# Optimization experiments

Measured on AMD Instinct MI355X. Metric: run time of the kernel, lower is better.

The kernel has to match this reference:

```python
import jax, jax.numpy as jnp
import numpy as np

NEG_SLOPE = 0.2
EPS = 1e-9


def setup_inputs() -> dict:
    key = jax.random.key(0)
    ks = jax.random.split(key, 6)
    B, N, E, H, F = 2, 40000, 640000, 4, 32
    X = jax.random.normal(ks[0], (B, N, H, F), dtype=jnp.float32)
    A_self = jax.random.normal(ks[1], (H, F), dtype=jnp.float32)
    A_adjc = jax.random.normal(ks[2], (H, F), dtype=jnp.float32)
    targets = jax.random.randint(ks[3], (B, E), 0, N, dtype=jnp.int32)
    sources = jax.random.randint(ks[4], (B, E), 0, N, dtype=jnp.int32)
    degree = jax.random.uniform(ks[5], (B, E), dtype=jnp.float32)
    return {"X": X, "A_self": A_self, "A_adjc": A_adjc, "degree": degree,
            "targets": targets, "sources": sources, "N": N}


def reference(X, A_self, A_adjc, degree, targets, sources, N):
    # X: [B, N, H, F]; targets/sources: [B, E]
    # per-node attention logits: [B, N, H]
    e_self = jnp.einsum("bnhf,hf->bnh", X, A_self)
    e_adjc = jnp.einsum("bnhf,hf->bnh", X, A_adjc)
    # gather to edges: [B, E, H]
    es = jnp.take_along_axis(e_self, targets[:, :, None], axis=1)
    ea = jnp.take_along_axis(e_adjc, sources[:, :, None], axis=1)
    e = jax.nn.leaky_relu(es + ea, negative_slope=NEG_SLOPE)

    seg_max = jax.vmap(lambda v, i: jax.ops.segment_max(v, i, num_segments=N))
    seg_sum = jax.vmap(lambda v, i: jax.ops.segment_sum(v, i, num_segments=N))

    # exact normalization from source: exp(e - seg_max(e)), then divide by
    # seg_max of the exponentials (+eps), both gathered back to edges.
    m1 = jnp.take_along_axis(seg_max(e, targets), targets[:, :, None], axis=1)
    e = jnp.exp(e - m1)
    m2 = jnp.take_along_axis(seg_max(e, targets), targets[:, :, None], axis=1)
    attn = (e / (m2 + EPS))[..., None]  # [B, E, H, 1]; dropout omitted (eval)

    # message passing: gather source features, weight, scatter-sum to targets
    msg = jnp.take_along_axis(X, sources[:, :, None, None], axis=1) * attn  # [B,E,H,F]
    out = seg_sum(msg, targets)  # [B, N, H, F]
    return out
```

## Files before the change

### kernel.cpp

```cpp
#include <hip/hip_runtime.h>
#include <stdint.h>

#define BB     2
#define NNODE  40000
#define NEDGE  640000
#define NH     4
#define NF     32
#define NHF    128
#define SEGN   (BB * NNODE)
#define GEDGE  (BB * NEDGE)
#define EC     16
#define SLOT   48

#define W      512
#define NBK_B  79
#define NBK    (BB * NBK_B)
#define CAP    9216
#define BLK_E  2048
#define NBLKA  (GEDGE / BLK_E)

static constexpr float NEG_SLOPE = 0.2f;
static constexpr float NEG_BIG   = -3.4e38f;

__global__ void prep_k(const float* __restrict__ X,
                       const float* __restrict__ As,
                       const float* __restrict__ Aa,
                       float* __restrict__ S, float* __restrict__ A,
                       unsigned* __restrict__ cursor) {
    int idx = blockIdx.x * blockDim.x + threadIdx.x;
    if (idx < NBK) cursor[idx] = 0u;
    if (idx >= SEGN * NH) return;
    int h = idx & (NH - 1);
    const float4* xv = (const float4*)(X + (size_t)idx * NF);
    const float4* sv = (const float4*)(As + h * NF);
    const float4* av = (const float4*)(Aa + h * NF);
    float s = 0.f, a = 0.f;
#pragma unroll
    for (int i = 0; i < 8; ++i) {
        float4 x = xv[i];
        float4 ws = sv[i];
        float4 wa = av[i];
        s += x.x * ws.x + x.y * ws.y + x.z * ws.z + x.w * ws.w;
        a += x.x * wa.x + x.y * wa.y + x.z * wa.z + x.w * wa.w;
    }
    S[idx] = s;
    A[idx] = a;
}

__global__ __launch_bounds__(256) void binA_k(const int* __restrict__ tg,
                                              const int* __restrict__ sc,
                                              unsigned* __restrict__ cursor,
                                              unsigned* __restrict__ pairs) {
    __shared__ unsigned hist[NBK];
    __shared__ unsigned lofs[NBK];
    __shared__ unsigned gofs[NBK];
    __shared__ unsigned wsum[4];
    __shared__ unsigned staged[BLK_E];
    __shared__ unsigned char sbk[BLK_E];
    int t = threadIdx.x;
    int base = blockIdx.x * BLK_E;
    for (int i = t; i < NBK; i += 256) hist[i] = 0u;
    __syncthreads();

    unsigned pr[8];
    unsigned short pbk[8], plp[8];
#pragma unroll
    for (int k = 0; k < 8; ++k) {
        int e = base + k * 256 + t;
        int tgv = tg[e], scv = sc[e];
        int b = (e >= NEDGE) ? 1 : 0;
        unsigned bk = (unsigned)(b * NBK_B + (tgv >> 9));
        pr[k]  = ((unsigned)(tgv & (W - 1)) << 16) | (unsigned)scv;
        pbk[k] = (unsigned short)bk;
        plp[k] = (unsigned short)atomicAdd(&hist[bk], 1u);
    }
    __syncthreads();
    {
        int lane = t & 63, w = t >> 6;
        unsigned v = (t < NBK) ? hist[t] : 0u;
        unsigned inc = v;
#pragma unroll
        for (int d = 1; d < 64; d <<= 1) {
            unsigned u = __shfl_up(inc, d);
            if (lane >= d) inc += u;
        }
        if (lane == 63) wsum[w] = inc;
        __syncthreads();
        unsigned woff = 0;
#pragma unroll
        for (int i = 0; i < 3; ++i) { if (i < w) woff += wsum[i]; }
        if (t < NBK) {
            lofs[t] = woff + inc - v;
            if (v > 0u)
                gofs[t] = atomicAdd(&cursor[t], v);
        }
    }
    __syncthreads();
#pragma unroll
    for (int k = 0; k < 8; ++k) {
        unsigned j = lofs[pbk[k]] + plp[k];
        staged[j] = pr[k];
        sbk[j] = (unsigned char)pbk[k];
    }
    __syncthreads();
    for (int j = t; j < BLK_E; j += 256) {
        unsigned bk = sbk[j];
        unsigned dst = gofs[bk] + ((unsigned)j - lofs[bk]);
        if (dst < CAP)
            pairs[(size_t)bk * CAP + dst] = staged[j];
    }
}

__global__ __launch_bounds__(1024) void binB_k(const unsigned* __restrict__ cursor,
                                               const unsigned* __restrict__ pairs,
                                               unsigned short* __restrict__ srt,
                                               unsigned* __restrict__ deg) {
    __shared__ unsigned short loc[W * SLOT];
    __shared__ unsigned dloc[W];
    int t = threadIdx.x;
    int gbk = blockIdx.x;
    int b = gbk / NBK_B;
    int bkloc = gbk - b * NBK_B;
    int node0 = b * NNODE + bkloc * W;
    int wEff = min(W, NNODE - bkloc * W);
    for (int i = t; i < W; i += 1024) dloc[i] = 0u;
    __syncthreads();
    int nE = (int)min(cursor[gbk], (unsigned)CAP);
    const unsigned* pb = pairs + (size_t)gbk * CAP;
    for (int j = t; j < nE; j += 1024) {
        unsigned p = pb[j];
        unsigned tl = p >> 16;
        unsigned pos = atomicAdd(&dloc[tl], 1u);
        if (pos < SLOT)
            loc[tl * SLOT + pos] = (unsigned short)(p & 0xFFFFu);
    }
    __syncthreads();
    unsigned* srt32 = (unsigned*)(srt + (size_t)node0 * SLOT);
    const unsigned* loc32 = (const unsigned*)loc;
    int n32 = wEff * SLOT / 2;
    for (int i = t; i < n32; i += 1024) srt32[i] = loc32[i];
    for (int i = t; i < wEff; i += 1024) deg[node0 + i] = dloc[i];
}

__global__ __launch_bounds__(256) void gather_k(
        const float* __restrict__ X, const float* __restrict__ S,
        const float* __restrict__ A, const unsigned* __restrict__ deg,
        const unsigned short* __restrict__ srt, float* __restrict__ OUT) {
    int node = blockIdx.x * 4 + (threadIdx.x >> 6);
    int t = threadIdx.x & 63;
    int hs = t & 3;
    int es = t >> 2;
    int h32 = t >> 5;
    int q = t & 31;
    int haq = q >> 3;
    int dg = min((int)deg[node], SLOT);
    int bbase = (node >= NNODE) ? NNODE : 0;
    size_t beg = (size_t)node * SLOT;

    float sh = S[node * NH + hs];
    float m_st = NEG_BIG;
    float m_ac = NEG_BIG;
    float4 acc = make_float4(0.f, 0.f, 0.f, 0.f);

    for (int c = 0; c < dg; c += EC) {
        int e = c + es;
        int sb = bbase;
        float v = NEG_BIG;
        if (e < dg) {
            sb = bbase + (int)srt[beg + e];
            v = sh + A[sb * NH + hs];
            v = v > 0.f ? v : NEG_SLOPE * v;
        }
        float m = v;
        m = fmaxf(m, __shfl_xor(m, 4));
        m = fmaxf(m, __shfl_xor(m, 8));
        m = fmaxf(m, __shfl_xor(m, 16));
        m = fmaxf(m, __shfl_xor(m, 32));
        m_st = fmaxf(m_st, m);
        float w = (e < dg) ? __expf(v - m_st) : 0.f;
        float ma_new = fmaxf(m_ac, __shfl(m, haq));
        float r = __expf(m_ac - ma_new);
        m_ac = ma_new;
        acc.x *= r; acc.y *= r; acc.z *= r; acc.w *= r;

        int cend = min(EC, dg - c);
        int npair = (cend + 1) >> 1;
#pragma unroll 8
        for (int i = 0; i < npair; ++i) {
            int e2 = 2 * i + h32;
            float we  = __shfl(w, 4 * e2 + haq);
            int   sbe = __shfl(sb, 4 * e2);
            const float4 x = *(const float4*)(X + (size_t)sbe * NHF + 4 * q);
            acc.x += x.x * we;
            acc.y += x.y * we;
            acc.z += x.z * we;
            acc.w += x.w * we;
        }
    }
    acc.x += __shfl_xor(acc.x, 32);
    acc.y += __shfl_xor(acc.y, 32);
    acc.z += __shfl_xor(acc.z, 32);
    acc.w += __shfl_xor(acc.w, 32);
    if (t < 32) {
        float4* o = (float4*)(OUT + (size_t)node * NHF + 4 * q);
        *o = acc;
    }
}

extern "C" void kernel_launch(void* const* d_in, const int* in_sizes, int n_in,
                              void* d_out, int out_size, void* d_ws, size_t ws_size,
                              hipStream_t stream) {
    const float* X  = (const float*)d_in[0];
    const float* As = (const float*)d_in[1];
    const float* Aa = (const float*)d_in[2];
    const int* tg = (const int*)d_in[4];
    const int* sc = (const int*)d_in[5];
    float* OUT = (float*)d_out;

    char* ws = (char*)d_ws;
    float*          S      = (float*)ws;
    float*          A      = (float*)(ws + 1280000);
    unsigned*       deg    = (unsigned*)(ws + 2560000);
    unsigned*       cursor = (unsigned*)(ws + 2880000);
    unsigned*       pairs  = (unsigned*)(ws + 2880640);
    unsigned short* srt    = (unsigned short*)(ws + 8705152);

    const int nlog = SEGN * NH;
    prep_k<<<(nlog + 255) / 256, 256, 0, stream>>>(X, As, Aa, S, A, cursor);
    binA_k<<<NBLKA, 256, 0, stream>>>(tg, sc, cursor, pairs);
    binB_k<<<NBK, 1024, 0, stream>>>(cursor, pairs, srt, deg);
    gather_k<<<SEGN / 4, 256, 0, stream>>>(X, S, A, deg, srt, OUT);
}
```

Baseline: 221.0 us.

## Precompute per-target softmax max with atomics and drop online rescaling in gather

Result: slower. 414.3 us (+87.4%).

```diff
diff --git a/kernel.cpp b/kernel.cpp
--- a/kernel.cpp
+++ b/kernel.cpp
@@ -9,7 +9,6 @@
 #define NHF    128
 #define SEGN   (BB * NNODE)
 #define GEDGE  (BB * NEDGE)
-#define EC     16
 #define SLOT   48
 
 #define W      512
@@ -20,16 +19,26 @@
 #define NBLKA  (GEDGE / BLK_E)
 
 static constexpr float NEG_SLOPE = 0.2f;
-static constexpr float NEG_BIG   = -3.4e38f;
+
+__device__ __forceinline__ unsigned fenc(float f) {
+    unsigned u = __float_as_uint(f);
+    return (u & 0x80000000u) ? ~u : (u | 0x80000000u);
+}
+__device__ __forceinline__ float fdec(unsigned e) {
+    unsigned u = (e & 0x80000000u) ? (e & 0x7FFFFFFFu) : ~e;
+    return __uint_as_float(u);
+}
 
 __global__ void prep_k(const float* __restrict__ X,
                        const float* __restrict__ As,
                        const float* __restrict__ Aa,
                        float* __restrict__ S, float* __restrict__ A,
-                       unsigned* __restrict__ cursor) {
+                       unsigned* __restrict__ cursor,
+                       unsigned* __restrict__ mpre) {
     int idx = blockIdx.x * blockDim.x + threadIdx.x;
     if (idx < NBK) cursor[idx] = 0u;
     if (idx >= SEGN * NH) return;
+    mpre[idx] = 0u;
     int h = idx & (NH - 1);
     const float4* xv = (const float4*)(X + (size_t)idx * NF);
     const float4* sv = (const float4*)(As + h * NF);
@@ -49,8 +58,11 @@
 
 __global__ __launch_bounds__(256) void binA_k(const int* __restrict__ tg,
                                               const int* __restrict__ sc,
+                                              const float* __restrict__ S,
+                                              const float* __restrict__ A,
                                               unsigned* __restrict__ cursor,
-                                              unsigned* __restrict__ pairs) {
+                                              unsigned* __restrict__ pairs,
+                                              unsigned* __restrict__ mpre) {
     __shared__ unsigned hist[NBK];
     __shared__ unsigned lofs[NBK];
     __shared__ unsigned gofs[NBK];
@@ -73,6 +85,19 @@
         pr[k]  = ((unsigned)(tgv & (W - 1)) << 16) | (unsigned)scv;
         pbk[k] = (unsigned short)bk;
         plp[k] = (unsigned short)atomicAdd(&hist[bk], 1u);
+        int tgg = b * NNODE + tgv;
+        int sgg = b * NNODE + scv;
+        float4 sv4 = *(const float4*)(S + (size_t)tgg * NH);
+        float4 av4 = *(const float4*)(A + (size_t)sgg * NH);
+        float v0 = sv4.x + av4.x; v0 = v0 > 0.f ? v0 : NEG_SLOPE * v0;
+        float v1 = sv4.y + av4.y; v1 = v1 > 0.f ? v1 : NEG_SLOPE * v1;
+        float v2 = sv4.z + av4.z; v2 = v2 > 0.f ? v2 : NEG_SLOPE * v2;
+        float v3 = sv4.w + av4.w; v3 = v3 > 0.f ? v3 : NEG_SLOPE * v3;
+        unsigned* mp = mpre + (size_t)tgg * NH;
+        atomicMax(mp + 0, fenc(v0));
+        atomicMax(mp + 1, fenc(v1));
+        atomicMax(mp + 2, fenc(v2));
+        atomicMax(mp + 3, fenc(v3));
     }
     __syncthreads();
     {
@@ -145,7 +170,8 @@
 __global__ __launch_bounds__(256) void gather_k(
         const float* __restrict__ X, const float* __restrict__ S,
         const float* __restrict__ A, const unsigned* __restrict__ deg,
-        const unsigned short* __restrict__ srt, float* __restrict__ OUT) {
+        const unsigned short* __restrict__ srt,
+        const unsigned* __restrict__ mpre, float* __restrict__ OUT) {
     int node = blockIdx.x * 4 + (threadIdx.x >> 6);
     int t = threadIdx.x & 63;
     int hs = t & 3;
@@ -158,38 +184,32 @@
     size_t beg = (size_t)node * SLOT;
 
     float sh = S[node * NH + hs];
-    float m_st = NEG_BIG;
-    float m_ac = NEG_BIG;
+    float mh = fdec(mpre[node * NH + hs]);
+
+    float w[3];
+    int   sb[3];
+#pragma unroll
+    for (int c = 0; c < 3; ++c) {
+        int e = 16 * c + es;
+        int s0 = bbase;
+        float wv = 0.f;
+        if (e < dg) {
+            s0 = bbase + (int)srt[beg + e];
+            float v = sh + A[s0 * NH + hs];
+            v = v > 0.f ? v : NEG_SLOPE * v;
+            wv = __expf(v - mh);
+        }
+        sb[c] = s0;
+        w[c]  = wv;
+    }
+
     float4 acc = make_float4(0.f, 0.f, 0.f, 0.f);
-
-    for (int c = 0; c < dg; c += EC) {
-        int e = c + es;
-        int sb = bbase;
-        float v = NEG_BIG;
-        if (e < dg) {
-            sb = bbase + (int)srt[beg + e];
-            v = sh + A[sb * NH + hs];
-            v = v > 0.f ? v : NEG_SLOPE * v;
-        }
-        float m = v;
-        m = fmaxf(m, __shfl_xor(m, 4));
-        m = fmaxf(m, __shfl_xor(m, 8));
-        m = fmaxf(m, __shfl_xor(m, 16));
-        m = fmaxf(m, __shfl_xor(m, 32));
-        m_st = fmaxf(m_st, m);
-        float w = (e < dg) ? __expf(v - m_st) : 0.f;
-        float ma_new = fmaxf(m_ac, __shfl(m, haq));
-        float r = __expf(m_ac - ma_new);
-        m_ac = ma_new;
-        acc.x *= r; acc.y *= r; acc.z *= r; acc.w *= r;
-
-        int cend = min(EC, dg - c);
-        int npair = (cend + 1) >> 1;
-#pragma unroll 8
-        for (int i = 0; i < npair; ++i) {
+#pragma unroll
+    for (int i = 0; i < 24; ++i) {
+        if (2 * i < dg) {
             int e2 = 2 * i + h32;
-            float we  = __shfl(w, 4 * e2 + haq);
-            int   sbe = __shfl(sb, 4 * e2);
+            float we  = __shfl(w[i >> 3],  4 * (e2 & 15) + haq);
+            int   sbe = __shfl(sb[i >> 3], 4 * (e2 & 15));
             const float4 x = *(const float4*)(X + (size_t)sbe * NHF + 4 * q);
             acc.x += x.x * we;
             acc.y += x.y * we;
@@ -224,10 +244,11 @@
     unsigned*       cursor = (unsigned*)(ws + 2880000);
     unsigned*       pairs  = (unsigned*)(ws + 2880640);
     unsigned short* srt    = (unsigned short*)(ws + 8705152);
+    unsigned*       mpre   = (unsigned*)(ws + 16385152);
 
     const int nlog = SEGN * NH;
-    prep_k<<<(nlog + 255) / 256, 256, 0, stream>>>(X, As, Aa, S, A, cursor);
-    binA_k<<<NBLKA, 256, 0, stream>>>(tg, sc, cursor, pairs);
+    prep_k<<<(nlog + 255) / 256, 256, 0, stream>>>(X, As, Aa, S, A, cursor, mpre);
+    binA_k<<<NBLKA, 256, 0, stream>>>(tg, sc, S, A, cursor, pairs, mpre);
     binB_k<<<NBK, 1024, 0, stream>>>(cursor, pairs, srt, deg);
-    gather_k<<<SEGN / 4, 256, 0, stream>>>(X, S, A, deg, srt, OUT);
-}
+    gather_k<<<SEGN / 4, 256, 0, stream>>>(X, S, A, deg, srt, mpre, OUT);
+}
```
